# Optimization experiments

Measured on AMD Instinct MI355X. Metric: run time of the kernel, lower is better.

## Reference

```python
import jax, jax.numpy as jnp
import numpy as np

N_EMBD = 384
NUM_HEADS = 6
HEAD_SIZE = 64
B, T = 64, 256


def setup_inputs() -> dict:
    key = jax.random.key(0)
    ks = jax.random.split(key, 6)
    s = 0.02
    x = jax.random.normal(ks[0], (B, T, N_EMBD), dtype=jnp.float32)
    # per-head projection weights, stored as [H, in, out] so y = x @ W
    Wq = jax.random.normal(ks[1], (NUM_HEADS, N_EMBD, HEAD_SIZE), dtype=jnp.float32) * s
    Wk = jax.random.normal(ks[2], (NUM_HEADS, N_EMBD, HEAD_SIZE), dtype=jnp.float32) * s
    Wv = jax.random.normal(ks[3], (NUM_HEADS, N_EMBD, HEAD_SIZE), dtype=jnp.float32) * s
    Wp = jax.random.normal(ks[4], (NUM_HEADS * HEAD_SIZE, N_EMBD), dtype=jnp.float32) * s
    bp = jax.random.normal(ks[5], (N_EMBD,), dtype=jnp.float32) * s
    return {"x": x, "Wq": Wq, "Wk": Wk, "Wv": Wv, "Wp": Wp, "bp": bp}


def reference(x, Wq, Wk, Wv, Wp, bp):
    # x: [B,T,C]; W{q,k,v}: [H,C,D]; dropout is identity (eval mode)
    Bb, Tt, _ = x.shape
    q = jnp.einsum('btc,hcd->bhtd', x, Wq)
    k = jnp.einsum('btc,hcd->bhtd', x, Wk)
    v = jnp.einsum('btc,hcd->bhtd', x, Wv)
    scale = HEAD_SIZE ** -0.5
    scores = jnp.einsum('bhtd,bhsd->bhts', q, k) * scale  # [B,H,T,T]
    causal = jnp.tril(jnp.ones((Tt, Tt), dtype=bool))
    scores = jnp.where(causal, scores, jnp.finfo(scores.dtype).min)
    attn = jax.nn.softmax(scores, axis=-1)
    out = jnp.einsum('bhts,bhsd->bhtd', attn, v)  # [B,H,T,D]
    out = out.transpose(0, 2, 1, 3).reshape(Bb, Tt, NUM_HEADS * HEAD_SIZE)
    return out @ Wp + bp
```

## Files before the change

kernel.cpp:

```cpp
#include <hip/hip_runtime.h>
#include <stdint.h>

#define B_  64
#define T_  256
#define C_  384
#define H_  6
#define D_  64
#define NTOK (B_*T_)

typedef float f32x4 __attribute__((ext_vector_type(4)));
typedef short s16x8 __attribute__((ext_vector_type(8)));

__device__ __forceinline__ unsigned short f2bf(float f) {
    unsigned int u;
    __builtin_memcpy(&u, &f, 4);
    u = u + 0x7FFFu + ((u >> 16) & 1u);
    return (unsigned short)(u >> 16);
}

__device__ __forceinline__ void async_copy16(const unsigned short* g, unsigned short* l) {
    __builtin_amdgcn_global_load_lds(
        (const __attribute__((address_space(1))) unsigned int*)g,
        (__attribute__((address_space(3))) unsigned int*)l, 16, 0, 0);
}

__global__ __launch_bounds__(256) void transpose_weights(
    const float* __restrict__ Wq, const float* __restrict__ Wk,
    const float* __restrict__ Wv, const float* __restrict__ Wp,
    unsigned short* __restrict__ W3, unsigned short* __restrict__ WTp) {
    __shared__ float tile[32][33];
    int z = blockIdx.y;
    const float* in;
    unsigned short* out;
    int R, Cc;
    if (z < 18) {
        int proj = z / 6, h = z % 6;
        const float* Wsrc = proj == 0 ? Wq : (proj == 1 ? Wk : Wv);
        in = Wsrc + h * C_ * D_;
        out = W3 + (size_t)(h * 192 + proj * 64) * C_;
        R = C_; Cc = D_;
    } else {
        in = Wp; out = WTp; R = C_; Cc = C_;
    }
    int tilesC = Cc / 32;
    int tilesR = R / 32;
    int bx = blockIdx.x;
    if (bx >= tilesC * tilesR) return;
    int tr = bx / tilesC, tc = bx % tilesC;
    int tx = threadIdx.x & 31;
    int ty8 = threadIdx.x >> 5;
    int gx = tc * 32 + tx;
#pragma unroll
    for (int i = 0; i < 4; i++) {
        int gy = tr * 32 + ty8 + i * 8;
        tile[ty8 + i * 8][tx] = in[gy * Cc + gx];
    }
    __syncthreads();
#pragma unroll
    for (int i = 0; i < 4; i++) {
        int oy = tc * 32 + ty8 + i * 8;
        int ox = tr * 32 + tx;
        out[oy * R + ox] = f2bf(tile[tx][ty8 + i * 8]);
    }
}

__global__ __launch_bounds__(1024, 4) void fused_attn(
    const float* __restrict__ X, const unsigned short* __restrict__ W3,
    unsigned short* __restrict__ Ows) {
    __shared__ alignas(16) unsigned short smem[67584];
    unsigned short* Wc     = smem;
    unsigned short* q_lds  = smem + 18432;
    unsigned short* k_lds  = q_lds + 16384;
    unsigned short* vT_lds = k_lds + 16384;

    int bh = blockIdx.x;
    int h = bh >> 6, b = bh & 63;
    int tid = threadIdx.x;
    int w = tid >> 6, lane = tid & 63;
    int n16 = lane & 15, q4 = lane >> 4;
    const int j = (w & 1) ? (15 - (w >> 1)) : (w >> 1);

    const unsigned short* W3h = W3 + (size_t)h * 192 * C_;
    const float* xb = X + (size_t)b * T_ * C_;

    f32x4 acc[12];
#pragma unroll
    for (int i = 0; i < 12; i++) acc[i] = (f32x4){0.f, 0.f, 0.f, 0.f};

    for (int kc = 0; kc < 4; kc++) {
        int ko = kc * 96;
        float4 a0[3], a1[3];
#pragma unroll
        for (int ks = 0; ks < 3; ks++) {
            const float* ap = xb + (size_t)(j * 16 + n16) * C_ + ko + ks * 32 + q4 * 8;
            a0[ks] = *reinterpret_cast<const float4*>(ap);
            a1[ks] = *reinterpret_cast<const float4*>(ap + 4);
        }
        if (kc) __syncthreads();
#pragma unroll
        for (int i = 0; i < 3; i++) {
            int sb = i * 1024 + w * 64;
            if (sb < 2304) {
                int L = sb + lane;
                int row = L / 12;
                int c = L % 12;
                int ks = c >> 2;
                int q4g = (c & 3) ^ (row & 3);
                async_copy16(W3h + (size_t)row * C_ + ko + ks * 32 + q4g * 8,
                             Wc + (size_t)sb * 8);
            }
        }
        __syncthreads();
#pragma unroll
        for (int ks = 0; ks < 3; ks++) {
            float4 lo = a0[ks], hi = a1[ks];
            s16x8 af;
            af[0] = (short)f2bf(lo.x); af[1] = (short)f2bf(lo.y);
            af[2] = (short)f2bf(lo.z); af[3] = (short)f2bf(lo.w);
            af[4] = (short)f2bf(hi.x); af[5] = (short)f2bf(hi.y);
            af[6] = (short)f2bf(hi.z); af[7] = (short)f2bf(hi.w);
#pragma unroll
            for (int ni = 0; ni < 12; ni++) {
                int row = ni * 16 + n16;
                int cp = ks * 4 + (q4 ^ (row & 3));
                s16x8 bf = *reinterpret_cast<const s16x8*>(&Wc[row * 96 + cp * 8]);
                if (ni < 8) {
                    acc[ni] = __builtin_amdgcn_mfma_f32_16x16x32_bf16(bf, af, acc[ni], 0, 0, 0);
                } else {
                    acc[ni] = __builtin_amdgcn_mfma_f32_16x16x32_bf16(af, bf, acc[ni], 0, 0, 0);
                }
            }
        }
    }
#pragma unroll
    for (int ni = 0; ni < 12; ni++) {
        ushort4 pk;
        pk.x = f2bf(acc[ni][0]); pk.y = f2bf(acc[ni][1]);
        pk.z = f2bf(acc[ni][2]); pk.w = f2bf(acc[ni][3]);
        if (ni < 8) {
            int t = j * 16 + n16;
            int cp = (2 * (ni & 3) + (q4 >> 1)) ^ (n16 & 7);
            unsigned short* dst = (ni < 4) ? q_lds : k_lds;
            *reinterpret_cast<ushort4*>(&dst[t * 64 + cp * 8 + (q4 & 1) * 4]) = pk;
        } else {
            int d = (ni - 8) * 16 + n16;
            int cp = (j * 2 + (q4 >> 1)) ^ (d & 7);
            *reinterpret_cast<ushort4*>(&vT_lds[d * 256 + cp * 8 + (q4 & 1) * 4]) = pk;
        }
    }
    __syncthreads();

    unsigned short* pw = smem + w * 640;
    const f32x4 zero4 = (f32x4){0.f, 0.f, 0.f, 0.f};

    {
        int t0 = j * 16;
        int tq = t0 + n16;
        s16x8 qa0 = *reinterpret_cast<const s16x8*>(&q_lds[tq * 64 + ((q4 ^ (n16 & 7)) * 8)]);
        s16x8 qa1 = *reinterpret_cast<const s16x8*>(&q_lds[tq * 64 + (((q4 + 4) ^ (n16 & 7)) * 8)]);

        f32x4 o[4];
        float l_lane[4];
#pragma unroll
        for (int i = 0; i < 4; i++) o[i] = zero4;
#pragma unroll
        for (int r = 0; r < 4; r++) l_lane[r] = 0.f;

        int nch = j / 2 + 1;
        for (int c = 0; c < nch; c++) {
            int s0 = c * 32;
            bool bAct = (s0 + 16) < (t0 + 16);
            int r0 = s0 + n16, r1 = s0 + 16 + n16;
            s16x8 k00 = *reinterpret_cast<const s16x8*>(&k_lds[r0 * 64 + ((q4 ^ (r0 & 7)) * 8)]);
            s16x8 k01 = *reinterpret_cast<const s16x8*>(&k_lds[r0 * 64 + (((q4 + 4) ^ (r0 & 7)) * 8)]);
            f32x4 sv0 = __builtin_amdgcn_mfma_f32_16x16x32_bf16(qa0, k00, zero4, 0, 0, 0);
            sv0 = __builtin_amdgcn_mfma_f32_16x16x32_bf16(qa1, k01, sv0, 0, 0, 0);
            f32x4 sv1 = zero4;
            if (bAct) {
                s16x8 k10 = *reinterpret_cast<const s16x8*>(&k_lds[r1 * 64 + ((q4 ^ (r1 & 7)) * 8)]);
                s16x8 k11 = *reinterpret_cast<const s16x8*>(&k_lds[r1 * 64 + (((q4 + 4) ^ (r1 & 7)) * 8)]);
                sv1 = __builtin_amdgcn_mfma_f32_16x16x32_bf16(qa0, k10, zero4, 0, 0, 0);
                sv1 = __builtin_amdgcn_mfma_f32_16x16x32_bf16(qa1, k11, sv1, 0, 0, 0);
            }
#pragma unroll
            for (int r = 0; r < 4; r++) {
                int t = t0 + q4 * 4 + r;
                float pA = (s0 + n16 <= t) ? __expf(sv0[r] * 0.125f) : 0.f;
                float pB = (bAct && (s0 + 16 + n16 <= t)) ? __expf(sv1[r] * 0.125f) : 0.f;
                l_lane[r] += pA + pB;
                pw[(q4 * 4 + r) * 40 + n16] = f2bf(pA);
                pw[(q4 * 4 + r) * 40 + 16 + n16] = f2bf(pB);
            }
            s16x8 pa = *reinterpret_cast<const s16x8*>(&pw[n16 * 40 + q4 * 8]);
#pragma unroll
            for (int dt = 0; dt < 4; dt++) {
                int d = dt * 16 + n16;
                int jp = (c * 4 + q4) ^ (d & 7);
                s16x8 vf = *reinterpret_cast<const s16x8*>(&vT_lds[d * 256 + jp * 8]);
                o[dt] = __builtin_amdgcn_mfma_f32_16x16x32_bf16(pa, vf, o[dt], 0, 0, 0);
            }
        }

        float linv[4];
#pragma unroll
        for (int r = 0; r < 4; r++) {
            float l = l_lane[r];
            l += __shfl_xor(l, 1);
            l += __shfl_xor(l, 2);
            l += __shfl_xor(l, 4);
            l += __shfl_xor(l, 8);
            linv[r] = 1.0f / l;
        }
#pragma unroll
        for (int dt = 0; dt < 4; dt++) {
            int col = h * 64 + dt * 16 + n16;
#pragma unroll
            for (int r = 0; r < 4; r++)
                Ows[(size_t)(b * T_ + t0 + q4 * 4 + r) * C_ + col] = f2bf(o[dt][r] * linv[r]);
        }
    }
}

__global__ __launch_bounds__(256) void gemm_out(
    const unsigned short* __restrict__ A, const unsigned short* __restrict__ WTp,
    const float* __restrict__ bp, float* __restrict__ out) {
    __shared__ alignas(16) unsigned short Bt[6 * 128 * 32];
    int m0 = blockIdx.x * 128;
    int n0 = blockIdx.y * 128;
    int tid = threadIdx.x;
    int w = tid >> 6, lane = tid & 63;
    int n16 = lane & 15, q4 = lane >> 4;

    f32x4 acc[2][8];
#pragma unroll
    for (int i = 0; i < 2; i++)
#pragma unroll
        for (int j = 0; j < 8; j++) acc[i][j] = (f32x4){0.f, 0.f, 0.f, 0.f};

    const unsigned short* a_base[2];
#pragma unroll
    for (int mi = 0; mi < 2; mi++)
        a_base[mi] = A + (size_t)(m0 + w * 32 + mi * 16 + n16) * C_ + q4 * 8;

    for (int half = 0; half < 2; half++) {
        int ko = half * 192;
        s16x8 af[2][6];
#pragma unroll
        for (int mi = 0; mi < 2; mi++)
#pragma unroll
            for (int ks = 0; ks < 6; ks++)
                af[mi][ks] = *reinterpret_cast<const s16x8*>(a_base[mi] + ko + ks * 32);
        if (half) __syncthreads();
#pragma unroll
        for (int i = 0; i < 12; i++) {
            int L = w * 768 + i * 64 + lane;
            int kstep = L >> 9;
            int rem = L & 511;
            int row = rem >> 2;
            int j = (rem & 3) ^ (row & 3);
            async_copy16(WTp + (size_t)(n0 + row) * C_ + ko + kstep * 32 + j * 8,
                         Bt + (size_t)(w * 768 + i * 64) * 8);
        }
        __syncthreads();
#pragma unroll
        for (int ks = 0; ks < 6; ks++) {
            s16x8 bf[8];
#pragma unroll
            for (int ni = 0; ni < 8; ni++) {
                int row = ni * 16 + n16;
                int jp = q4 ^ (row & 3);
                bf[ni] = *reinterpret_cast<const s16x8*>(&Bt[ks * 4096 + row * 32 + jp * 8]);
            }
#pragma unroll
            for (int mi = 0; mi < 2; mi++)
#pragma unroll
                for (int ni = 0; ni < 8; ni++)
                    acc[mi][ni] = __builtin_amdgcn_mfma_f32_16x16x32_bf16(
                        bf[ni], af[mi][ks], acc[mi][ni], 0, 0, 0);
        }
    }

#pragma unroll
    for (int mi = 0; mi < 2; mi++) {
        int tr = m0 + w * 32 + mi * 16 + n16;
#pragma unroll
        for (int ni = 0; ni < 8; ni++) {
            int c0 = n0 + ni * 16 + q4 * 4;
            float4 bias = *reinterpret_cast<const float4*>(&bp[c0]);
            float4 res;
            res.x = acc[mi][ni][0] + bias.x;
            res.y = acc[mi][ni][1] + bias.y;
            res.z = acc[mi][ni][2] + bias.z;
            res.w = acc[mi][ni][3] + bias.w;
            *reinterpret_cast<float4*>(&out[(size_t)tr * C_ + c0]) = res;
        }
    }
}

extern "C" void kernel_launch(void* const* d_in, const int* in_sizes, int n_in,
                              void* d_out, int out_size, void* d_ws, size_t ws_size,
                              hipStream_t stream) {
    const float* x  = (const float*)d_in[0];
    const float* Wq = (const float*)d_in[1];
    const float* Wk = (const float*)d_in[2];
    const float* Wv = (const float*)d_in[3];
    const float* Wp = (const float*)d_in[4];
    const float* bp = (const float*)d_in[5];
    float* out = (float*)d_out;

    char* ws = (char*)d_ws;
    size_t off = 0;
    auto alloc = [&](size_t bytes) -> unsigned short* {
        unsigned short* p = (unsigned short*)(ws + off);
        off += (bytes + 255) & ~(size_t)255;
        return p;
    };
    unsigned short* W3  = alloc((size_t)H_ * 192 * C_ * 2);
    unsigned short* WTp = alloc((size_t)C_ * C_ * 2);
    unsigned short* Ows = alloc((size_t)NTOK * C_ * 2);

    transpose_weights<<<dim3(144, 19), dim3(256), 0, stream>>>(
        Wq, Wk, Wv, Wp, W3, WTp);
    fused_attn<<<dim3(B_ * H_), dim3(1024), 0, stream>>>(x, W3, Ows);
    gemm_out<<<dim3(128, 3), dim3(256), 0, stream>>>(Ows, WTp, bp, out);
}
```

Measured before the change: 151.6 us.

## Use 32x32x16 MFMA tiles for fused QKV projection stage

Reworks the QKV projection inside the fused attention kernel. Each wave now computes a 32-token by 96-column slab with three 32x32x16 bf16 MFMAs, where before it computed 16 tokens by 192 columns with twelve 16x16x32 MFMAs. Pairs of waves share the same 32 token rows and split the Q/K/V output columns. The intent is to raise math per LDS weight fragment and cut instruction count. In exchange, each thread now loads twice as many X float4 values per k-chunk, and the epilogue swizzle mapping into q/k/vT LDS has to match exactly what the attention stage expects.

```diff
diff --git a/kernel.cpp b/kernel.cpp
--- a/kernel.cpp
+++ b/kernel.cpp
@@ -8,8 +8,9 @@
 #define D_  64
 #define NTOK (B_*T_)
 
-typedef float f32x4 __attribute__((ext_vector_type(4)));
-typedef short s16x8 __attribute__((ext_vector_type(8)));
+typedef float f32x4  __attribute__((ext_vector_type(4)));
+typedef float f32x16 __attribute__((ext_vector_type(16)));
+typedef short s16x8  __attribute__((ext_vector_type(8)));
 
 __device__ __forceinline__ unsigned short f2bf(float f) {
     unsigned int u;
@@ -78,23 +79,27 @@
     int tid = threadIdx.x;
     int w = tid >> 6, lane = tid & 63;
     int n16 = lane & 15, q4 = lane >> 4;
+    int m32 = lane & 31, kh = lane >> 5;
+    int g = w >> 1, ch = w & 1;
     const int j = (w & 1) ? (15 - (w >> 1)) : (w >> 1);
 
     const unsigned short* W3h = W3 + (size_t)h * 192 * C_;
     const float* xb = X + (size_t)b * T_ * C_;
 
-    f32x4 acc[12];
-#pragma unroll
-    for (int i = 0; i < 12; i++) acc[i] = (f32x4){0.f, 0.f, 0.f, 0.f};
+    f32x16 acc[3];
+#pragma unroll
+    for (int i = 0; i < 3; i++)
+#pragma unroll
+        for (int e = 0; e < 16; e++) acc[i][e] = 0.f;
 
     for (int kc = 0; kc < 4; kc++) {
         int ko = kc * 96;
-        float4 a0[3], a1[3];
-#pragma unroll
-        for (int ks = 0; ks < 3; ks++) {
-            const float* ap = xb + (size_t)(j * 16 + n16) * C_ + ko + ks * 32 + q4 * 8;
-            a0[ks] = *reinterpret_cast<const float4*>(ap);
-            a1[ks] = *reinterpret_cast<const float4*>(ap + 4);
+        float4 a[12];
+#pragma unroll
+        for (int ks = 0; ks < 6; ks++) {
+            const float* ap = xb + (size_t)(g * 32 + m32) * C_ + ko + ks * 16 + kh * 8;
+            a[2 * ks]     = *reinterpret_cast<const float4*>(ap);
+            a[2 * ks + 1] = *reinterpret_cast<const float4*>(ap + 4);
         }
         if (kc) __syncthreads();
 #pragma unroll
@@ -112,40 +117,49 @@
         }
         __syncthreads();
 #pragma unroll
-        for (int ks = 0; ks < 3; ks++) {
-            float4 lo = a0[ks], hi = a1[ks];
+        for (int ks = 0; ks < 6; ks++) {
+            float4 lo = a[2 * ks], hi = a[2 * ks + 1];
             s16x8 af;
             af[0] = (short)f2bf(lo.x); af[1] = (short)f2bf(lo.y);
             af[2] = (short)f2bf(lo.z); af[3] = (short)f2bf(lo.w);
             af[4] = (short)f2bf(hi.x); af[5] = (short)f2bf(hi.y);
             af[6] = (short)f2bf(hi.z); af[7] = (short)f2bf(hi.w);
-#pragma unroll
-            for (int ni = 0; ni < 12; ni++) {
-                int row = ni * 16 + n16;
-                int cp = ks * 4 + (q4 ^ (row & 3));
-                s16x8 bf = *reinterpret_cast<const s16x8*>(&Wc[row * 96 + cp * 8]);
-                if (ni < 8) {
-                    acc[ni] = __builtin_amdgcn_mfma_f32_16x16x32_bf16(bf, af, acc[ni], 0, 0, 0);
-                } else {
-                    acc[ni] = __builtin_amdgcn_mfma_f32_16x16x32_bf16(af, bf, acc[ni], 0, 0, 0);
-                }
-            }
-        }
-    }
-#pragma unroll
-    for (int ni = 0; ni < 12; ni++) {
-        ushort4 pk;
-        pk.x = f2bf(acc[ni][0]); pk.y = f2bf(acc[ni][1]);
-        pk.z = f2bf(acc[ni][2]); pk.w = f2bf(acc[ni][3]);
-        if (ni < 8) {
-            int t = j * 16 + n16;
-            int cp = (2 * (ni & 3) + (q4 >> 1)) ^ (n16 & 7);
-            unsigned short* dst = (ni < 4) ? q_lds : k_lds;
-            *reinterpret_cast<ushort4*>(&dst[t * 64 + cp * 8 + (q4 & 1) * 4]) = pk;
-        } else {
-            int d = (ni - 8) * 16 + n16;
-            int cp = (j * 2 + (q4 >> 1)) ^ (d & 7);
-            *reinterpret_cast<ushort4*>(&vT_lds[d * 256 + cp * 8 + (q4 & 1) * 4]) = pk;
+            int idx8 = ks * 2 + kh;
+#pragma unroll
+            for (int nt_l = 0; nt_l < 3; nt_l++) {
+                int nt = ch * 3 + nt_l;
+                int row = nt * 32 + m32;
+                int c = (idx8 & ~3) | ((idx8 & 3) ^ (row & 3));
+                s16x8 bf = *reinterpret_cast<const s16x8*>(&Wc[row * 96 + c * 8]);
+                if (nt < 4)
+                    acc[nt_l] = __builtin_amdgcn_mfma_f32_32x32x16_bf16(bf, af, acc[nt_l], 0, 0, 0);
+                else
+                    acc[nt_l] = __builtin_amdgcn_mfma_f32_32x32x16_bf16(af, bf, acc[nt_l], 0, 0, 0);
+            }
+        }
+    }
+#pragma unroll
+    for (int nt_l = 0; nt_l < 3; nt_l++) {
+        int nt = ch * 3 + nt_l;
+#pragma unroll
+        for (int rg = 0; rg < 4; rg++) {
+            ushort4 pk;
+            pk.x = f2bf(acc[nt_l][rg * 4 + 0]);
+            pk.y = f2bf(acc[nt_l][rg * 4 + 1]);
+            pk.z = f2bf(acc[nt_l][rg * 4 + 2]);
+            pk.w = f2bf(acc[nt_l][rg * 4 + 3]);
+            if (nt < 4) {
+                int t = g * 32 + m32;
+                int lc = (nt & 1) * 4 + rg;
+                int cp = lc ^ (lane & 7);
+                unsigned short* dst = (nt < 2) ? q_lds : k_lds;
+                *reinterpret_cast<ushort4*>(&dst[t * 64 + cp * 8 + kh * 4]) = pk;
+            } else {
+                int d = (nt - 4) * 32 + m32;
+                int jc = g * 4 + rg;
+                int jp = jc ^ (lane & 7);
+                *reinterpret_cast<ushort4*>(&vT_lds[d * 256 + jp * 8 + kh * 4]) = pk;
+            }
         }
     }
     __syncthreads();
```

Measured after the change: 180.7 us. +19.2%, slower.
